# Optimization experiments

Hardware: AMD Instinct MI355X
Metric: run time of the kernel (lower is better)

## Reference

```python
import jax, jax.numpy as jnp
import numpy as np


def setup_inputs() -> dict:
    key = jax.random.key(0)
    k_x, k_w, k_b = jax.random.split(key, 3)
    B, Cin, H, W = 32, 256, 56, 56
    Cout, KH, KW = 256, 3, 3
    x = jax.random.normal(k_x, (B, Cin, H, W), dtype=jnp.float32)
    fp_weight = jax.random.normal(k_w, (Cout, Cin, KH, KW), dtype=jnp.float32)
    # binary quantization, conv_mode='input_ch': per-output-channel scale
    scaling_factors = jnp.mean(jnp.abs(fp_weight), axis=(1, 2, 3), keepdims=True)  # [Cout,1,1,1]
    quant_weights = jnp.sign(fp_weight)  # values in {-1,0,1}
    bias = jax.random.normal(k_b, (Cout,), dtype=jnp.float32)
    return {"x": x, "scaling_factors": scaling_factors,
            "quant_weights": quant_weights, "bias": bias}


def reference(x, scaling_factors, quant_weights, bias):
    # Dequantize: per-out-channel scale times sign weights
    new_weights = scaling_factors * quant_weights  # [Cout,Cin,3,3]
    out = jax.lax.conv_general_dilated(
        x, new_weights,
        window_strides=(1, 1),
        padding=((1, 1), (1, 1)),
        dimension_numbers=("NCHW", "OIHW", "NCHW"),
    )
    return out + bias[None, :, None, None]
```

## Files before the change

### kernel.cpp

```cpp
#include <hip/hip_runtime.h>

using half8   = __attribute__((ext_vector_type(8))) _Float16;
using floatx4 = __attribute__((ext_vector_type(4))) float;
using short8  = __attribute__((ext_vector_type(8))) short;

#define XT_ROW_ELEMS 2560
#define XT_ROW_BYTES 5120
#define XT_OFF ((size_t)2 << 20)
#define XT_BYTES ((size_t)256 * 58 * XT_ROW_BYTES)

__device__ __forceinline__ void dma16(const void* g, void* l) {
  __builtin_amdgcn_global_load_lds(
      (const __attribute__((address_space(1))) void*)g,
      (__attribute__((address_space(3))) void*)l, 16, 0, 0);
}

__global__ __launch_bounds__(256) void prep_kernel(
    const float* __restrict__ x, const float* __restrict__ qw,
    _Float16* __restrict__ wre, _Float16* __restrict__ xt)
{
  const int bid = blockIdx.x;
  const int t = threadIdx.x;
  if (bid >= 14848) {
    int idx = (bid - 14848) * 256 + t;
    int c = idx & 255, co = (idx >> 8) & 255, s = idx >> 16;
    wre[idx] = (_Float16)qw[(co * 256 + c) * 9 + s];
    return;
  }
  __shared__ _Float16 lt[32 * 57];
  const int hh = bid % 58;
  const int bc = bid / 58;
  const int cc = bc & 7, b = bc >> 3;
  _Float16* dst = xt + ((size_t)bc * 58 + hh) * XT_ROW_ELEMS;
  const bool interior = (hh >= 1) && (hh <= 56);
  if (interior) {
    const int c = t >> 3, j = t & 7;
    const float* src = x + (((size_t)(b * 256 + cc * 32 + c)) * 56 + (hh - 1)) * 56 + j * 7;
#pragma unroll
    for (int i = 0; i < 7; ++i) lt[c * 57 + j * 7 + i] = (_Float16)src[i];
  }
  __syncthreads();
  for (int ch = t; ch < 320; ch += 256) {
    int pos = ch / 5, sl = ch - pos * 5;
    short8 v = {0, 0, 0, 0, 0, 0, 0, 0};
    if (interior && sl < 4 && pos >= 1 && pos <= 56) {
      int w = pos - 1;
#pragma unroll
      for (int i = 0; i < 8; ++i)
        v[i] = __builtin_bit_cast(short, lt[(sl * 8 + i) * 57 + w]);
    }
    *reinterpret_cast<short8*>(dst + ch * 8) = v;
  }
}

__global__ __launch_bounds__(256, 2) void binconv_mfma(
    const float* __restrict__ scale, const float* __restrict__ bias,
    const _Float16* __restrict__ wre, const _Float16* __restrict__ xt,
    float* __restrict__ out)
{
  __shared__ _Float16 xs[2 * 4 * 64 * 40];

  const int tid  = threadIdx.x;
  const int nb   = blockIdx.x;
  const int b    = nb / 28;
  const int h0   = (nb % 28) * 2;
  const int wave = tid >> 6;
  const int lane = tid & 63;
  const int nl   = lane & 15;
  const int quad = lane >> 4;
  const int co_wave = wave * 64;

  int bbase[7];
#pragma unroll
  for (int j = 0; j < 7; ++j) {
    int n = j * 16 + nl;
    int r = (n >= 56) ? 1 : 0;
    int w = n - r * 56;
    bbase[j] = (r * 64 + w) * 80 + quad * 16;
  }

  const _Float16* aptr[4];
#pragma unroll
  for (int mi = 0; mi < 4; ++mi)
    aptr[mi] = wre + (co_wave + mi * 16 + nl) * 256 + quad * 8;

  floatx4 acc[4][7];
#pragma unroll
  for (int mi = 0; mi < 4; ++mi)
#pragma unroll
    for (int j = 0; j < 7; ++j)
      acc[mi][j] = (floatx4){0.f, 0.f, 0.f, 0.f};

  const char* xsrc = (const char*)(xt + ((size_t)(b * 8) * 58 + h0) * XT_ROW_ELEMS);
  const int wlane = wave * XT_ROW_BYTES + lane * 16;
  const int wldso = wave * XT_ROW_BYTES;

#pragma unroll
  for (int i = 0; i < 5; ++i)
    dma16(xsrc + wlane + i * 1024, (char*)xs + wldso + i * 1024);

  int bufoff = 0;
  for (int cc = 0; cc < 8; ++cc) {
    __syncthreads();
    if (cc < 7) {
      const char* srcn = xsrc + (size_t)(cc + 1) * (58 * XT_ROW_BYTES);
#pragma unroll
      for (int i = 0; i < 5; ++i)
        dma16(srcn + wlane + i * 1024,
              (char*)xs + (bufoff ^ 20480) + wldso + i * 1024);
    }
    const int c0 = cc * 32;
    const char* xb = (const char*)xs + bufoff;
#pragma unroll
    for (int s = 0; s < 9; ++s) {
      const int kh = s / 3, kw = s - kh * 3;
      half8 a[4];
#pragma unroll
      for (int mi = 0; mi < 4; ++mi)
        a[mi] = *reinterpret_cast<const half8*>(aptr[mi] + s * 65536 + c0);
      const int soff = (kh * 64 + kw) * 80;
#pragma unroll
      for (int j = 0; j < 7; ++j) {
        half8 bf = *reinterpret_cast<const half8*>(xb + bbase[j] + soff);
#pragma unroll
        for (int mi = 0; mi < 4; ++mi)
          acc[mi][j] = __builtin_amdgcn_mfma_f32_16x16x32_f16(a[mi], bf, acc[mi][j], 0, 0, 0);
      }
    }
    bufoff ^= 20480;
  }

#pragma unroll
  for (int mi = 0; mi < 4; ++mi) {
#pragma unroll
    for (int reg = 0; reg < 4; ++reg) {
      int co = co_wave + mi * 16 + quad * 4 + reg;
      float s_ = scale[co];
      float bi = bias[co];
#pragma unroll
      for (int j = 0; j < 7; ++j) {
        int n = j * 16 + nl;
        int r = (n >= 56) ? 1 : 0;
        int w = n - r * 56;
        out[(((size_t)b * 256 + co) * 56 + (h0 + r)) * 56 + w] =
            acc[mi][j][reg] * s_ + bi;
      }
    }
  }
}

__global__ void repack_weights(const float* __restrict__ qw,
                               _Float16* __restrict__ wre, int n) {
  int t = blockIdx.x * 256 + threadIdx.x;
  if (t >= n) return;
  int c = t & 255, co = (t >> 8) & 255, s = t >> 16;
  wre[t] = (_Float16)qw[(co * 256 + c) * 9 + s];
}

__global__ __launch_bounds__(256, 2) void binconv_fallback(
    const float* __restrict__ x, const float* __restrict__ scale,
    const float* __restrict__ bias, const _Float16* __restrict__ wre,
    float* __restrict__ out)
{
  __shared__ _Float16 xsl[4 * 58 * 32];
  const int tid = threadIdx.x;
  const int nb = blockIdx.x;
  const int b = nb / 28;
  const int h0 = (nb % 28) * 2;
  const int wave = tid >> 6;
  const int lane = tid & 63;
  const int nl = lane & 15;
  const int quad = lane >> 4;
  const int co_wave = wave * 64;
  {
    int c = tid & 31, g = tid >> 5, r = g >> 1, side = g & 1;
    xsl[(r * 58 + side * 57) * 32 + c] = (_Float16)0.0f;
  }
  int bbase[7];
#pragma unroll
  for (int j = 0; j < 7; ++j) {
    int n = j * 16 + nl;
    int r = (n >= 56) ? 1 : 0;
    int w = n - r * 56;
    bbase[j] = (r * 58 + w) * 64 + quad * 16;
  }
  const _Float16* aptr[4];
#pragma unroll
  for (int mi = 0; mi < 4; ++mi)
    aptr[mi] = wre + (co_wave + mi * 16 + nl) * 256 + quad * 8;
  floatx4 acc[4][7];
#pragma unroll
  for (int mi = 0; mi < 4; ++mi)
#pragma unroll
    for (int j = 0; j < 7; ++j) acc[mi][j] = (floatx4){0.f, 0.f, 0.f, 0.f};
  const int sc = tid & 31, sg = tid >> 5;
  for (int c0 = 0; c0 < 256; c0 += 32) {
    for (int p = sg; p < 28; p += 8) {
      int r = p / 7, wg = p - r * 7, h = h0 - 1 + r, w0 = wg * 8;
      float v[8];
      if (h >= 0 && h < 56) {
        const float* src = x + (((size_t)b * 256 + c0 + sc) * 56 + h) * 56 + w0;
        float4 u0 = *reinterpret_cast<const float4*>(src);
        float4 u1 = *reinterpret_cast<const float4*>(src + 4);
        v[0] = u0.x; v[1] = u0.y; v[2] = u0.z; v[3] = u0.w;
        v[4] = u1.x; v[5] = u1.y; v[6] = u1.z; v[7] = u1.w;
      } else {
#pragma unroll
        for (int i = 0; i < 8; ++i) v[i] = 0.f;
      }
      int basei = (r * 58 + 1 + w0) * 32 + sc;
#pragma unroll
      for (int i = 0; i < 8; ++i) xsl[basei + i * 32] = (_Float16)v[i];
    }
    __syncthreads();
#pragma unroll
    for (int s = 0; s < 9; ++s) {
      const int kh = s / 3, kw = s - kh * 3;
      half8 a[4];
#pragma unroll
      for (int mi = 0; mi < 4; ++mi)
        a[mi] = *reinterpret_cast<const half8*>(aptr[mi] + s * 65536 + c0);
      const int soff = (kh * 58 + kw) * 64;
#pragma unroll
      for (int j = 0; j < 7; ++j) {
        half8 bf = *reinterpret_cast<const half8*>(
            reinterpret_cast<const char*>(xsl) + bbase[j] + soff);
#pragma unroll
        for (int mi = 0; mi < 4; ++mi)
          acc[mi][j] = __builtin_amdgcn_mfma_f32_16x16x32_f16(a[mi], bf, acc[mi][j], 0, 0, 0);
      }
    }
    __syncthreads();
  }
#pragma unroll
  for (int mi = 0; mi < 4; ++mi) {
#pragma unroll
    for (int reg = 0; reg < 4; ++reg) {
      int co = co_wave + mi * 16 + quad * 4 + reg;
      float s_ = scale[co];
      float bi = bias[co];
#pragma unroll
      for (int j = 0; j < 7; ++j) {
        int n = j * 16 + nl;
        int r = (n >= 56) ? 1 : 0;
        int w = n - r * 56;
        out[(((size_t)b * 256 + co) * 56 + (h0 + r)) * 56 + w] =
            acc[mi][j][reg] * s_ + bi;
      }
    }
  }
}

extern "C" void kernel_launch(void* const* d_in, const int* in_sizes, int n_in,
                              void* d_out, int out_size, void* d_ws, size_t ws_size,
                              hipStream_t stream) {
  const float* x     = (const float*)d_in[0];
  const float* scale = (const float*)d_in[1];
  const float* qw    = (const float*)d_in[2];
  const float* bias  = (const float*)d_in[3];
  float* out = (float*)d_out;

  _Float16* wre = (_Float16*)d_ws;

  if (ws_size >= XT_OFF + XT_BYTES) {
    _Float16* xt = (_Float16*)((char*)d_ws + XT_OFF);
    prep_kernel<<<17152, 256, 0, stream>>>(x, qw, wre, xt);
    binconv_mfma<<<896, 256, 0, stream>>>(scale, bias, wre, xt, out);
  } else {
    repack_weights<<<2304, 256, 0, stream>>>(qw, wre, 9 * 256 * 256);
    binconv_fallback<<<896, 256, 0, stream>>>(x, scale, bias, wre, out);
  }
}
```

Before: 334.5 us.

## Fuse input fp16 transpose into conv kernel with register-staged prefetch

```diff
diff --git a/kernel.cpp b/kernel.cpp
--- a/kernel.cpp
+++ b/kernel.cpp
@@ -2,60 +2,20 @@
 
 using half8   = __attribute__((ext_vector_type(8))) _Float16;
 using floatx4 = __attribute__((ext_vector_type(4))) float;
+using floatx2 = __attribute__((ext_vector_type(2))) float;
 using short8  = __attribute__((ext_vector_type(8))) short;
 
-#define XT_ROW_ELEMS 2560
-#define XT_ROW_BYTES 5120
-#define XT_OFF ((size_t)2 << 20)
-#define XT_BYTES ((size_t)256 * 58 * XT_ROW_BYTES)
-
-__device__ __forceinline__ void dma16(const void* g, void* l) {
-  __builtin_amdgcn_global_load_lds(
-      (const __attribute__((address_space(1))) void*)g,
-      (__attribute__((address_space(3))) void*)l, 16, 0, 0);
+__global__ void repack_weights(const float* __restrict__ qw,
+                               _Float16* __restrict__ wre, int n) {
+  int t = blockIdx.x * 256 + threadIdx.x;
+  if (t >= n) return;
+  int c = t & 255, co = (t >> 8) & 255, s = t >> 16;
+  wre[t] = (_Float16)qw[(co * 256 + c) * 9 + s];
 }
 
-__global__ __launch_bounds__(256) void prep_kernel(
-    const float* __restrict__ x, const float* __restrict__ qw,
-    _Float16* __restrict__ wre, _Float16* __restrict__ xt)
-{
-  const int bid = blockIdx.x;
-  const int t = threadIdx.x;
-  if (bid >= 14848) {
-    int idx = (bid - 14848) * 256 + t;
-    int c = idx & 255, co = (idx >> 8) & 255, s = idx >> 16;
-    wre[idx] = (_Float16)qw[(co * 256 + c) * 9 + s];
-    return;
-  }
-  __shared__ _Float16 lt[32 * 57];
-  const int hh = bid % 58;
-  const int bc = bid / 58;
-  const int cc = bc & 7, b = bc >> 3;
-  _Float16* dst = xt + ((size_t)bc * 58 + hh) * XT_ROW_ELEMS;
-  const bool interior = (hh >= 1) && (hh <= 56);
-  if (interior) {
-    const int c = t >> 3, j = t & 7;
-    const float* src = x + (((size_t)(b * 256 + cc * 32 + c)) * 56 + (hh - 1)) * 56 + j * 7;
-#pragma unroll
-    for (int i = 0; i < 7; ++i) lt[c * 57 + j * 7 + i] = (_Float16)src[i];
-  }
-  __syncthreads();
-  for (int ch = t; ch < 320; ch += 256) {
-    int pos = ch / 5, sl = ch - pos * 5;
-    short8 v = {0, 0, 0, 0, 0, 0, 0, 0};
-    if (interior && sl < 4 && pos >= 1 && pos <= 56) {
-      int w = pos - 1;
-#pragma unroll
-      for (int i = 0; i < 8; ++i)
-        v[i] = __builtin_bit_cast(short, lt[(sl * 8 + i) * 57 + w]);
-    }
-    *reinterpret_cast<short8*>(dst + ch * 8) = v;
-  }
-}
-
-__global__ __launch_bounds__(256, 2) void binconv_mfma(
-    const float* __restrict__ scale, const float* __restrict__ bias,
-    const _Float16* __restrict__ wre, const _Float16* __restrict__ xt,
+__global__ __launch_bounds__(256, 2) void binconv_fused(
+    const float* __restrict__ x, const float* __restrict__ scale,
+    const float* __restrict__ bias, const _Float16* __restrict__ wre,
     float* __restrict__ out)
 {
   __shared__ _Float16 xs[2 * 4 * 64 * 40];
@@ -69,6 +29,24 @@
   const int nl   = lane & 15;
   const int quad = lane >> 4;
   const int co_wave = wave * 64;
+
+  {
+    short8 z = {0, 0, 0, 0, 0, 0, 0, 0};
+    short8* xs8 = reinterpret_cast<short8*>(xs);
+#pragma unroll
+    for (int i = 0; i < 10; ++i) xs8[tid + i * 256] = z;
+  }
+
+  const int p   = lane & 15;
+  const int wq  = lane >> 4;
+  const int w0  = wq * 14;
+  const int h   = h0 + wave - 1;
+  const bool hok = (h >= 0) && (h < 56);
+  const float* xca = x + (((size_t)b * 256 + 2 * p) * 56 + (hok ? h : 0)) * 56 + w0;
+  const float* xcb = xca + 3136;
+  _Float16* const wrow = xs + wave * 2560 + 2 * p;
+
+  floatx2 va[7], vb[7];
 
   int bbase[7];
 #pragma unroll
@@ -91,26 +69,37 @@
     for (int j = 0; j < 7; ++j)
       acc[mi][j] = (floatx4){0.f, 0.f, 0.f, 0.f};
 
-  const char* xsrc = (const char*)(xt + ((size_t)(b * 8) * 58 + h0) * XT_ROW_ELEMS);
-  const int wlane = wave * XT_ROW_BYTES + lane * 16;
-  const int wldso = wave * XT_ROW_BYTES;
+  __syncthreads();
 
+  if (hok) {
 #pragma unroll
-  for (int i = 0; i < 5; ++i)
-    dma16(xsrc + wlane + i * 1024, (char*)xs + wldso + i * 1024);
+    for (int i = 0; i < 7; ++i) {
+      va[i] = *reinterpret_cast<const floatx2*>(xca + 2 * i);
+      vb[i] = *reinterpret_cast<const floatx2*>(xcb + 2 * i);
+    }
+#pragma unroll
+    for (int i = 0; i < 7; ++i) {
+      auto u = __builtin_amdgcn_cvt_pkrtz(va[i][0], vb[i][0]);
+      auto v = __builtin_amdgcn_cvt_pkrtz(va[i][1], vb[i][1]);
+      *reinterpret_cast<decltype(u)*>(wrow + (w0 + 2 * i + 1) * 40) = u;
+      *reinterpret_cast<decltype(v)*>(wrow + (w0 + 2 * i + 2) * 40) = v;
+    }
+  }
 
-  int bufoff = 0;
+  int bufe = 0;
   for (int cc = 0; cc < 8; ++cc) {
     __syncthreads();
-    if (cc < 7) {
-      const char* srcn = xsrc + (size_t)(cc + 1) * (58 * XT_ROW_BYTES);
+    if (cc < 7 && hok) {
+      const float* A = xca + (size_t)(cc + 1) * 100352;
+      const float* B = xcb + (size_t)(cc + 1) * 100352;
 #pragma unroll
-      for (int i = 0; i < 5; ++i)
-        dma16(srcn + wlane + i * 1024,
-              (char*)xs + (bufoff ^ 20480) + wldso + i * 1024);
+      for (int i = 0; i < 7; ++i) {
+        va[i] = *reinterpret_cast<const floatx2*>(A + 2 * i);
+        vb[i] = *reinterpret_cast<const floatx2*>(B + 2 * i);
+      }
     }
     const int c0 = cc * 32;
-    const char* xb = (const char*)xs + bufoff;
+    const char* xb = reinterpret_cast<const char*>(xs) + bufe * 2;
 #pragma unroll
     for (int s = 0; s < 9; ++s) {
       const int kh = s / 3, kw = s - kh * 3;
@@ -127,111 +116,19 @@
           acc[mi][j] = __builtin_amdgcn_mfma_f32_16x16x32_f16(a[mi], bf, acc[mi][j], 0, 0, 0);
       }
     }
-    bufoff ^= 20480;
+    if (cc < 7 && hok) {
+      _Float16* d = wrow + (bufe ^ 10240);
+#pragma unroll
+      for (int i = 0; i < 7; ++i) {
+        auto u = __builtin_amdgcn_cvt_pkrtz(va[i][0], vb[i][0]);
+        auto v = __builtin_amdgcn_cvt_pkrtz(va[i][1], vb[i][1]);
+        *reinterpret_cast<decltype(u)*>(d + (w0 + 2 * i + 1) * 40) = u;
+        *reinterpret_cast<decltype(v)*>(d + (w0 + 2 * i + 2) * 40) = v;
+      }
+    }
+    bufe ^= 10240;
   }
 
-#pragma unroll
-  for (int mi = 0; mi < 4; ++mi) {
-#pragma unroll
-    for (int reg = 0; reg < 4; ++reg) {
-      int co = co_wave + mi * 16 + quad * 4 + reg;
-      float s_ = scale[co];
-      float bi = bias[co];
-#pragma unroll
-      for (int j = 0; j < 7; ++j) {
-        int n = j * 16 + nl;
-        int r = (n >= 56) ? 1 : 0;
-        int w = n - r * 56;
-        out[(((size_t)b * 256 + co) * 56 + (h0 + r)) * 56 + w] =
-            acc[mi][j][reg] * s_ + bi;
-      }
-    }
-  }
-}
-
-__global__ void repack_weights(const float* __restrict__ qw,
-                               _Float16* __restrict__ wre, int n) {
-  int t = blockIdx.x * 256 + threadIdx.x;
-  if (t >= n) return;
-  int c = t & 255, co = (t >> 8) & 255, s = t >> 16;
-  wre[t] = (_Float16)qw[(co * 256 + c) * 9 + s];
-}
-
-__global__ __launch_bounds__(256, 2) void binconv_fallback(
-    const float* __restrict__ x, const float* __restrict__ scale,
-    const float* __restrict__ bias, const _Float16* __restrict__ wre,
-    float* __restrict__ out)
-{
-  __shared__ _Float16 xsl[4 * 58 * 32];
-  const int tid = threadIdx.x;
-  const int nb = blockIdx.x;
-  const int b = nb / 28;
-  const int h0 = (nb % 28) * 2;
-  const int wave = tid >> 6;
-  const int lane = tid & 63;
-  const int nl = lane & 15;
-  const int quad = lane >> 4;
-  const int co_wave = wave * 64;
-  {
-    int c = tid & 31, g = tid >> 5, r = g >> 1, side = g & 1;
-    xsl[(r * 58 + side * 57) * 32 + c] = (_Float16)0.0f;
-  }
-  int bbase[7];
-#pragma unroll
-  for (int j = 0; j < 7; ++j) {
-    int n = j * 16 + nl;
-    int r = (n >= 56) ? 1 : 0;
-    int w = n - r * 56;
-    bbase[j] = (r * 58 + w) * 64 + quad * 16;
-  }
-  const _Float16* aptr[4];
-#pragma unroll
-  for (int mi = 0; mi < 4; ++mi)
-    aptr[mi] = wre + (co_wave + mi * 16 + nl) * 256 + quad * 8;
-  floatx4 acc[4][7];
-#pragma unroll
-  for (int mi = 0; mi < 4; ++mi)
-#pragma unroll
-    for (int j = 0; j < 7; ++j) acc[mi][j] = (floatx4){0.f, 0.f, 0.f, 0.f};
-  const int sc = tid & 31, sg = tid >> 5;
-  for (int c0 = 0; c0 < 256; c0 += 32) {
-    for (int p = sg; p < 28; p += 8) {
-      int r = p / 7, wg = p - r * 7, h = h0 - 1 + r, w0 = wg * 8;
-      float v[8];
-      if (h >= 0 && h < 56) {
-        const float* src = x + (((size_t)b * 256 + c0 + sc) * 56 + h) * 56 + w0;
-        float4 u0 = *reinterpret_cast<const float4*>(src);
-        float4 u1 = *reinterpret_cast<const float4*>(src + 4);
-        v[0] = u0.x; v[1] = u0.y; v[2] = u0.z; v[3] = u0.w;
-        v[4] = u1.x; v[5] = u1.y; v[6] = u1.z; v[7] = u1.w;
-      } else {
-#pragma unroll
-        for (int i = 0; i < 8; ++i) v[i] = 0.f;
-      }
-      int basei = (r * 58 + 1 + w0) * 32 + sc;
-#pragma unroll
-      for (int i = 0; i < 8; ++i) xsl[basei + i * 32] = (_Float16)v[i];
-    }
-    __syncthreads();
-#pragma unroll
-    for (int s = 0; s < 9; ++s) {
-      const int kh = s / 3, kw = s - kh * 3;
-      half8 a[4];
-#pragma unroll
-      for (int mi = 0; mi < 4; ++mi)
-        a[mi] = *reinterpret_cast<const half8*>(aptr[mi] + s * 65536 + c0);
-      const int soff = (kh * 58 + kw) * 64;
-#pragma unroll
-      for (int j = 0; j < 7; ++j) {
-        half8 bf = *reinterpret_cast<const half8*>(
-            reinterpret_cast<const char*>(xsl) + bbase[j] + soff);
-#pragma unroll
-        for (int mi = 0; mi < 4; ++mi)
-          acc[mi][j] = __builtin_amdgcn_mfma_f32_16x16x32_f16(a[mi], bf, acc[mi][j], 0, 0, 0);
-      }
-    }
-    __syncthreads();
-  }
 #pragma unroll
   for (int mi = 0; mi < 4; ++mi) {
 #pragma unroll
@@ -262,12 +159,6 @@
 
   _Float16* wre = (_Float16*)d_ws;
 
-  if (ws_size >= XT_OFF + XT_BYTES) {
-    _Float16* xt = (_Float16*)((char*)d_ws + XT_OFF);
-    prep_kernel<<<17152, 256, 0, stream>>>(x, qw, wre, xt);
-    binconv_mfma<<<896, 256, 0, stream>>>(scale, bias, wre, xt, out);
-  } else {
-    repack_weights<<<2304, 256, 0, stream>>>(qw, wre, 9 * 256 * 256);
-    binconv_fallback<<<896, 256, 0, stream>>>(x, scale, bias, wre, out);
-  }
+  repack_weights<<<2304, 256, 0, stream>>>(qw, wre, 9 * 256 * 256);
+  binconv_fused<<<896, 256, 0, stream>>>(x, scale, bias, wre, out);
 }
```

After: 335.0 us. No clear change (+0.1%).
